# Kernel tuning notes

Measured on AMD Instinct MI355X. Metric: run time of the kernel, lower is better.

The kernel has to match this reference:

```python
import jax, jax.numpy as jnp
import numpy as np

VOCAB = 1276   # medical-code vocab (one_hot depth for word)
AGE_DEPTH = 91 # one_hot depth for age


def setup_inputs() -> dict:
    key = jax.random.key(0)
    k1, k2, k3 = jax.random.split(key, 3)
    B, S, BAG, D = 64, 128, 40, 768
    word = jax.random.randint(k1, (B, S, BAG), 0, VOCAB)
    age = jax.random.randint(k2, (B, S), 0, AGE_DEPTH)
    W = jax.random.normal(k3, (VOCAB + AGE_DEPTH, D), dtype=jnp.float32) * 0.02
    b = jnp.zeros((D,), dtype=jnp.float32)
    return {"word": word, "age": age, "W": W, "b": b}


def reference(word, age, W, b):
    # word: [B, S, BAG] int codes; age: [B, S] int.
    B, S, BAG = word.shape
    # Multi-hot count-sum: equivalent to reduce_sum(one_hot(word, VOCAB), axis=-2)
    # but computed via scatter-add, avoiding the dense [B,S,BAG,VOCAB] tensor.
    flat = word.reshape(B * S, BAG)
    offs = jnp.arange(B * S, dtype=word.dtype)[:, None] * VOCAB
    counts = (
        jnp.zeros((B * S * VOCAB,), jnp.float32)
        .at[(flat + offs).ravel()]
        .add(1.0)
        .reshape(B, S, VOCAB)
    )
    year = jax.nn.one_hot(age, AGE_DEPTH, dtype=jnp.float32)  # [B, S, 91]
    x = jnp.concatenate([counts, year], axis=-1)              # [B, S, 1367]
    return x @ W + b                                          # [B, S, 768]
```

## Files before the change

### kernel.cpp

```cpp
#include <hip/hip_runtime.h>
#include <hip/hip_fp16.h>

constexpr int BAG       = 40;
constexpr int D         = 768;
constexpr int VOCAB     = 1276;
constexpr int AGE_DEPTH = 91;
constexpr int WROWS     = VOCAB + AGE_DEPTH;

constexpr int ROWS_PB = 256;
constexpr int TPB     = 512;
constexpr int COLS    = 16;
constexpr int SPB     = 6;
constexpr int CPB     = COLS * SPB;
constexpr int NSG     = D / CPB;
constexpr int LDSU    = 2 * WROWS;
constexpr int SITER   = (LDSU + TPB - 1) / TPB;

typedef float fx4 __attribute__((ext_vector_type(4)));

__device__ __forceinline__ __half2 u2h(uint u) {
    union { uint u; __half2 h; } v; v.u = u; return v.h;
}
__device__ __forceinline__ ushort f2h(float f) {
    __half h = __float2half(f);
    return *reinterpret_cast<ushort*>(&h);
}
__device__ __forceinline__ uint4 pack8(const float4 a, const float4 b) {
    uint4 p;
    p.x = (uint)f2h(a.x) | ((uint)f2h(a.y) << 16);
    p.y = (uint)f2h(a.z) | ((uint)f2h(a.w) << 16);
    p.z = (uint)f2h(b.x) | ((uint)f2h(b.y) << 16);
    p.w = (uint)f2h(b.z) | ((uint)f2h(b.w) << 16);
    return p;
}

__global__ __launch_bounds__(TPB) void embed_dbuf_kernel(
    const int* __restrict__ word,
    const int* __restrict__ age,
    const float* __restrict__ W,
    const float* __restrict__ bias,
    float* __restrict__ out)
{
    __shared__ uint4 buf[2][LDSU];

    const int rb  = blockIdx.x;
    const int cb0 = blockIdx.y * CPB;

    const int t     = threadIdx.x;
    const int chunk = t & 1;
    const int rloc  = t >> 1;
    const int row   = rb * ROWS_PB + rloc;

    const int* __restrict__ wrow = word + row * BAG;
    int idx[BAG];
    #pragma unroll
    for (int j = 0; j < BAG; j += 4) {
        const int4 q = *reinterpret_cast<const int4*>(wrow + j);
        idx[j] = q.x; idx[j + 1] = q.y; idx[j + 2] = q.z; idx[j + 3] = q.w;
    }
    const int aidx = VOCAB + age[row];

    #pragma unroll
    for (int k = 0; k < SITER; ++k) {
        const int i = t + k * TPB;
        if (i < LDSU) {
            const int r = i >> 1, u = i & 1;
            const float* src = W + (size_t)r * D + cb0 + u * 8;
            const float4 a = *reinterpret_cast<const float4*>(src);
            const float4 b = *reinterpret_cast<const float4*>(src + 4);
            buf[0][u * WROWS + r] = pack8(a, b);
        }
    }
    __syncthreads();

    #pragma unroll
    for (int s = 0; s < SPB; ++s) {
        float4 sa[SITER], sb[SITER];
        if (s + 1 < SPB) {
            const int cbn = cb0 + (s + 1) * COLS;
            #pragma unroll
            for (int k = 0; k < SITER; ++k) {
                const int i = t + k * TPB;
                if (i < LDSU) {
                    const int r = i >> 1, u = i & 1;
                    const float* src = W + (size_t)r * D + cbn + u * 8;
                    sa[k] = *reinterpret_cast<const float4*>(src);
                    sb[k] = *reinterpret_cast<const float4*>(src + 4);
                }
            }
        }

        const uint4* __restrict__ lp = buf[s & 1] + chunk * WROWS;
        __half2 a0 = u2h(0u), a1 = u2h(0u), a2 = u2h(0u), a3 = u2h(0u);
        #pragma unroll
        for (int kb = 0; kb < 5; ++kb) {
            uint4 g[8];
            #pragma unroll
            for (int u = 0; u < 8; ++u)
                g[u] = lp[idx[kb * 8 + u]];
            #pragma unroll
            for (int u = 0; u < 8; ++u) {
                a0 = __hadd2(a0, u2h(g[u].x));
                a1 = __hadd2(a1, u2h(g[u].y));
                a2 = __hadd2(a2, u2h(g[u].z));
                a3 = __hadd2(a3, u2h(g[u].w));
            }
        }
        {
            const uint4 g = lp[aidx];
            a0 = __hadd2(a0, u2h(g.x));
            a1 = __hadd2(a1, u2h(g.y));
            a2 = __hadd2(a2, u2h(g.z));
            a3 = __hadd2(a3, u2h(g.w));
        }

        {
            const int c = cb0 + s * COLS + chunk * 8;
            const float4 b0 = *reinterpret_cast<const float4*>(bias + c);
            const float4 b1 = *reinterpret_cast<const float4*>(bias + c + 4);
            fx4 o0 = { b0.x + __low2float(a0), b0.y + __high2float(a0),
                       b0.z + __low2float(a1), b0.w + __high2float(a1) };
            fx4 o1 = { b1.x + __low2float(a2), b1.y + __high2float(a2),
                       b1.z + __low2float(a3), b1.w + __high2float(a3) };
            float* op = out + (size_t)row * D + c;
            __builtin_nontemporal_store(o0, reinterpret_cast<fx4*>(op));
            __builtin_nontemporal_store(o1, reinterpret_cast<fx4*>(op + 4));
        }

        if (s + 1 < SPB) {
            #pragma unroll
            for (int k = 0; k < SITER; ++k) {
                const int i = t + k * TPB;
                if (i < LDSU) {
                    const int r = i >> 1, u = i & 1;
                    buf[(s + 1) & 1][u * WROWS + r] = pack8(sa[k], sb[k]);
                }
            }
        }
        __syncthreads();
    }
}

__global__ __launch_bounds__(192) void embedbag_f32_kernel(
    const int* __restrict__ word, const int* __restrict__ age,
    const float* __restrict__ W, const float* __restrict__ bias,
    float* __restrict__ out)
{
    const int row = blockIdx.x;
    const int c   = threadIdx.x * 4;

    float4 acc = *reinterpret_cast<const float4*>(&bias[c]);
    const int* __restrict__ wrow = word + row * BAG;

    #pragma unroll 8
    for (int j = 0; j < BAG; ++j) {
        const int idx = wrow[j];
        const float4 v = *reinterpret_cast<const float4*>(&W[(size_t)idx * D + c]);
        acc.x += v.x; acc.y += v.y; acc.z += v.z; acc.w += v.w;
    }
    {
        const int idx = VOCAB + age[row];
        const float4 v = *reinterpret_cast<const float4*>(&W[(size_t)idx * D + c]);
        acc.x += v.x; acc.y += v.y; acc.z += v.z; acc.w += v.w;
    }
    *reinterpret_cast<float4*>(&out[(size_t)row * D + c]) = acc;
}

extern "C" void kernel_launch(void* const* d_in, const int* in_sizes, int n_in,
                              void* d_out, int out_size, void* d_ws, size_t ws_size,
                              hipStream_t stream) {
    const int* word   = (const int*)d_in[0];
    const int* age    = (const int*)d_in[1];
    const float* W    = (const float*)d_in[2];
    const float* bias = (const float*)d_in[3];
    float* out        = (float*)d_out;

    const int rows = in_sizes[1];

    if (rows % ROWS_PB == 0) {
        dim3 grid(rows / ROWS_PB, NSG);
        embed_dbuf_kernel<<<grid, TPB, 0, stream>>>(word, age, W, bias, out);
    } else {
        embedbag_f32_kernel<<<rows, D / 4, 0, stream>>>(word, age, W, bias, out);
    }
}
```

Before: 29.37 us.

## Split rows between LDS-staged fp16 gather waves and direct fp32 gather waves

Replaces the double-buffered multi-slice kernel with a warp-specialized one. Six waves per block stage a single 16-column fp16 slice of W in LDS and gather-sum 384 rows in two groups. The other two waves handle the remaining rows (the tail beyond 7680) by gathering full fp32 rows directly from global memory. The grid becomes 48 slices times 20 bands with an occupancy hint of 6 blocks, aiming to balance work and drop the per-slice restaging and barriers. The split depends on the row count matching the fixed band sizes, and it mixes fp16 and fp32 accumulation across rows.

```diff
diff --git a/kernel.cpp b/kernel.cpp
--- a/kernel.cpp
+++ b/kernel.cpp
@@ -7,14 +7,15 @@
 constexpr int AGE_DEPTH = 91;
 constexpr int WROWS     = VOCAB + AGE_DEPTH;
 
-constexpr int ROWS_PB = 256;
-constexpr int TPB     = 512;
-constexpr int COLS    = 16;
-constexpr int SPB     = 6;
-constexpr int CPB     = COLS * SPB;
-constexpr int NSG     = D / CPB;
-constexpr int LDSU    = 2 * WROWS;
-constexpr int SITER   = (LDSU + TPB - 1) / TPB;
+constexpr int COLS       = 16;
+constexpr int NSLC       = D / COLS;
+constexpr int BANDS      = 20;
+constexpr int GPB        = 2;
+constexpr int GROUP_ROWS = 192;
+constexpr int ROWS_A     = BANDS * GPB * GROUP_ROWS;
+constexpr int TPB        = 512;
+constexpr int NA         = 384;
+constexpr int LDSU       = 2 * WROWS;
 
 typedef float fx4 __attribute__((ext_vector_type(4)));
 
@@ -34,90 +35,75 @@
     return p;
 }
 
-__global__ __launch_bounds__(TPB) void embed_dbuf_kernel(
+__global__ __launch_bounds__(TPB, 6) void embed_dual_kernel(
     const int* __restrict__ word,
     const int* __restrict__ age,
     const float* __restrict__ W,
     const float* __restrict__ bias,
-    float* __restrict__ out)
+    float* __restrict__ out,
+    int rows)
 {
-    __shared__ uint4 buf[2][LDSU];
-
-    const int rb  = blockIdx.x;
-    const int cb0 = blockIdx.y * CPB;
-
+    __shared__ uint4 lds4[LDSU];
+
+    const int bid   = blockIdx.x;
+    const int slice = bid % NSLC;
+    const int band  = bid / NSLC;
+    const int c0    = slice * COLS;
     const int t     = threadIdx.x;
-    const int chunk = t & 1;
-    const int rloc  = t >> 1;
-    const int row   = rb * ROWS_PB + rloc;
-
-    const int* __restrict__ wrow = word + row * BAG;
-    int idx[BAG];
-    #pragma unroll
-    for (int j = 0; j < BAG; j += 4) {
-        const int4 q = *reinterpret_cast<const int4*>(wrow + j);
-        idx[j] = q.x; idx[j + 1] = q.y; idx[j + 2] = q.z; idx[j + 3] = q.w;
-    }
-    const int aidx = VOCAB + age[row];
-
-    #pragma unroll
-    for (int k = 0; k < SITER; ++k) {
-        const int i = t + k * TPB;
-        if (i < LDSU) {
-            const int r = i >> 1, u = i & 1;
-            const float* src = W + (size_t)r * D + cb0 + u * 8;
-            const float4 a = *reinterpret_cast<const float4*>(src);
-            const float4 b = *reinterpret_cast<const float4*>(src + 4);
-            buf[0][u * WROWS + r] = pack8(a, b);
+
+    if (t < NA) {
+        #pragma unroll
+        for (int k = 0; k < 8; ++k) {
+            const int i = t + k * NA;
+            if (i < LDSU) {
+                const int r = i >> 1, u = i & 1;
+                const float* src = W + (size_t)r * D + c0 + u * 8;
+                const float4 a = *reinterpret_cast<const float4*>(src);
+                const float4 b = *reinterpret_cast<const float4*>(src + 4);
+                lds4[u * WROWS + r] = pack8(a, b);
+            }
         }
     }
     __syncthreads();
 
-    #pragma unroll
-    for (int s = 0; s < SPB; ++s) {
-        float4 sa[SITER], sb[SITER];
-        if (s + 1 < SPB) {
-            const int cbn = cb0 + (s + 1) * COLS;
+    if (t < NA) {
+        const int rloc  = t >> 1;
+        const int chunk = t & 1;
+        const uint4* __restrict__ lp = lds4 + chunk * WROWS;
+        const int c = c0 + chunk * 8;
+        const float4 b0 = *reinterpret_cast<const float4*>(bias + c);
+        const float4 b1 = *reinterpret_cast<const float4*>(bias + c + 4);
+
+        #pragma unroll
+        for (int gi = 0; gi < GPB; ++gi) {
+            const int row = (band * GPB + gi) * GROUP_ROWS + rloc;
+            const int* __restrict__ wrow = word + row * BAG;
+            const int aidx = VOCAB + age[row];
+
+            __half2 a0 = u2h(0u), a1 = u2h(0u), a2 = u2h(0u), a3 = u2h(0u);
             #pragma unroll
-            for (int k = 0; k < SITER; ++k) {
-                const int i = t + k * TPB;
-                if (i < LDSU) {
-                    const int r = i >> 1, u = i & 1;
-                    const float* src = W + (size_t)r * D + cbn + u * 8;
-                    sa[k] = *reinterpret_cast<const float4*>(src);
-                    sb[k] = *reinterpret_cast<const float4*>(src + 4);
+            for (int kb = 0; kb < 5; ++kb) {
+                const int4 q0 = *reinterpret_cast<const int4*>(wrow + kb * 8);
+                const int4 q1 = *reinterpret_cast<const int4*>(wrow + kb * 8 + 4);
+                const int id[8] = {q0.x, q0.y, q0.z, q0.w, q1.x, q1.y, q1.z, q1.w};
+                uint4 g[8];
+                #pragma unroll
+                for (int u = 0; u < 8; ++u) g[u] = lp[id[u]];
+                #pragma unroll
+                for (int u = 0; u < 8; ++u) {
+                    a0 = __hadd2(a0, u2h(g[u].x));
+                    a1 = __hadd2(a1, u2h(g[u].y));
+                    a2 = __hadd2(a2, u2h(g[u].z));
+                    a3 = __hadd2(a3, u2h(g[u].w));
                 }
             }
-        }
-
-        const uint4* __restrict__ lp = buf[s & 1] + chunk * WROWS;
-        __half2 a0 = u2h(0u), a1 = u2h(0u), a2 = u2h(0u), a3 = u2h(0u);
-        #pragma unroll
-        for (int kb = 0; kb < 5; ++kb) {
-            uint4 g[8];
-            #pragma unroll
-            for (int u = 0; u < 8; ++u)
-                g[u] = lp[idx[kb * 8 + u]];
-            #pragma unroll
-            for (int u = 0; u < 8; ++u) {
-                a0 = __hadd2(a0, u2h(g[u].x));
-                a1 = __hadd2(a1, u2h(g[u].y));
-                a2 = __hadd2(a2, u2h(g[u].z));
-                a3 = __hadd2(a3, u2h(g[u].w));
-            }
-        }
-        {
-            const uint4 g = lp[aidx];
-            a0 = __hadd2(a0, u2h(g.x));
-            a1 = __hadd2(a1, u2h(g.y));
-            a2 = __hadd2(a2, u2h(g.z));
-            a3 = __hadd2(a3, u2h(g.w));
-        }
-
-        {
-            const int c = cb0 + s * COLS + chunk * 8;
-            const float4 b0 = *reinterpret_cast<const float4*>(bias + c);
-            const float4 b1 = *reinterpret_cast<const float4*>(bias + c + 4);
+            {
+                const uint4 g = lp[aidx];
+                a0 = __hadd2(a0, u2h(g.x));
+                a1 = __hadd2(a1, u2h(g.y));
+                a2 = __hadd2(a2, u2h(g.z));
+                a3 = __hadd2(a3, u2h(g.w));
+            }
             fx4 o0 = { b0.x + __low2float(a0), b0.y + __high2float(a0),
                        b0.z + __low2float(a1), b0.w + __high2float(a1) };
             fx4 o1 = { b1.x + __low2float(a2), b1.y + __high2float(a2),
@@ -126,18 +112,56 @@
             __builtin_nontemporal_store(o0, reinterpret_cast<fx4*>(op));
             __builtin_nontemporal_store(o1, reinterpret_cast<fx4*>(op + 4));
         }
-
-        if (s + 1 < SPB) {
-            #pragma unroll
-            for (int k = 0; k < SITER; ++k) {
-                const int i = t + k * TPB;
-                if (i < LDSU) {
-                    const int r = i >> 1, u = i & 1;
-                    buf[(s + 1) & 1][u * WROWS + r] = pack8(sa[k], sb[k]);
-                }
-            }
+    } else {
+        const int w    = (t >> 6) - 6;
+        const int lane = t & 63;
+        const int slot = bid * 2 + w;
+        const int row  = ROWS_A + slot;
+        if (row < rows) {
+            const int* __restrict__ wrow = word + row * BAG;
+            const int aidx = VOCAB + age[row];
+            const int cb = lane * 4;
+
+            float4 acc0 = *reinterpret_cast<const float4*>(bias + cb);
+            float4 acc1 = *reinterpret_cast<const float4*>(bias + 256 + cb);
+            float4 acc2 = *reinterpret_cast<const float4*>(bias + 512 + cb);
+
+            #pragma unroll 4
+            for (int j = 0; j < BAG; j += 2) {
+                const int ia = wrow[j];
+                const int ib = wrow[j + 1];
+                const float* pa = W + (size_t)ia * D + cb;
+                const float* pb = W + (size_t)ib * D + cb;
+                const float4 a0 = *reinterpret_cast<const float4*>(pa);
+                const float4 a1 = *reinterpret_cast<const float4*>(pa + 256);
+                const float4 a2 = *reinterpret_cast<const float4*>(pa + 512);
+                const float4 v0 = *reinterpret_cast<const float4*>(pb);
+                const float4 v1 = *reinterpret_cast<const float4*>(pb + 256);
+                const float4 v2 = *reinterpret_cast<const float4*>(pb + 512);
+                acc0.x += a0.x + v0.x; acc0.y += a0.y + v0.y;
+                acc0.z += a0.z + v0.z; acc0.w += a0.w + v0.w;
+                acc1.x += a1.x + v1.x; acc1.y += a1.y + v1.y;
+                acc1.z += a1.z + v1.z; acc1.w += a1.w + v1.w;
+                acc2.x += a2.x + v2.x; acc2.y += a2.y + v2.y;
+                acc2.z += a2.z + v2.z; acc2.w += a2.w + v2.w;
+            }
+            {
+                const float* pa = W + (size_t)aidx * D + cb;
+                const float4 a0 = *reinterpret_cast<const float4*>(pa);
+                const float4 a1 = *reinterpret_cast<const float4*>(pa + 256);
+                const float4 a2 = *reinterpret_cast<const float4*>(pa + 512);
+                acc0.x += a0.x; acc0.y += a0.y; acc0.z += a0.z; acc0.w += a0.w;
+                acc1.x += a1.x; acc1.y += a1.y; acc1.z += a1.z; acc1.w += a1.w;
+                acc2.x += a2.x; acc2.y += a2.y; acc2.z += a2.z; acc2.w += a2.w;
+            }
+            float* op = out + (size_t)row * D + cb;
+            fx4 o0 = {acc0.x, acc0.y, acc0.z, acc0.w};
+            fx4 o1 = {acc1.x, acc1.y, acc1.z, acc1.w};
+            fx4 o2 = {acc2.x, acc2.y, acc2.z, acc2.w};
+            __builtin_nontemporal_store(o0, reinterpret_cast<fx4*>(op));
+            __builtin_nontemporal_store(o1, reinterpret_cast<fx4*>(op + 256));
+            __builtin_nontemporal_store(o2, reinterpret_cast<fx4*>(op + 512));
         }
-        __syncthreads();
     }
 }
 
@@ -177,9 +201,10 @@
 
     const int rows = in_sizes[1];
 
-    if (rows % ROWS_PB == 0) {
-        dim3 grid(rows / ROWS_PB, NSG);
-        embed_dbuf_kernel<<<grid, TPB, 0, stream>>>(word, age, W, bias, out);
+    const int rows_b = rows - ROWS_A;
+    if (rows_b > 0 && rows_b <= 2 * NSLC * BANDS) {
+        embed_dual_kernel<<<NSLC * BANDS, TPB, 0, stream>>>(
+            word, age, W, bias, out, rows);
     } else {
         embedbag_f32_kernel<<<rows, D / 4, 0, stream>>>(word, age, W, bias, out);
     }
```

After: 29.39 us. Within noise of the previous version (+0.1%).
